# Kernel optimization log

Measured on AMD Instinct MI355X. Metric: run time of the kernel, lower is better.

Reference implementation:

```python
import jax, jax.numpy as jnp
import numpy as np
from jax import lax

B, C, H, W = 32, 256, 56, 56

def _conv(x, w, stride, groups=1, pad='VALID'):
    return lax.conv_general_dilated(x, w, (stride, stride), pad,
                                    feature_group_count=groups,
                                    dimension_numbers=('NCHW', 'OIHW', 'NCHW'))

def _ln(x, g, b, eps=1e-5):
    mu = jnp.mean(x, -1, keepdims=True)
    var = jnp.mean((x - mu) ** 2, -1, keepdims=True)
    return (x - mu) * lax.rsqrt(var + eps) * g + b

def setup_inputs() -> dict:
    key = jax.random.key(0)
    ks = jax.random.split(key, 16)
    s = 0.02
    Ch = C // 2
    d = {}
    d['x'] = jax.random.normal(ks[0], (B, C, H, W), jnp.float32)
    d['Wq'] = jax.random.normal(ks[1], (C, C), jnp.float32) * s;  d['bq'] = jnp.zeros((C,), jnp.float32)
    d['Wk'] = jax.random.normal(ks[2], (C, C), jnp.float32) * s;  d['bk'] = jnp.zeros((C,), jnp.float32)
    d['Wv'] = jax.random.normal(ks[3], (C, C), jnp.float32) * s;  d['bv'] = jnp.zeros((C,), jnp.float32)
    d['sr1_w'] = jax.random.normal(ks[4], (C, C, 8, 8), jnp.float32) * s; d['sr1_b'] = jnp.zeros((C,), jnp.float32)
    d['ln1_g'] = jnp.ones((C,), jnp.float32); d['ln1_b'] = jnp.zeros((C,), jnp.float32)
    d['sr2_w'] = jax.random.normal(ks[5], (C, C, 4, 4), jnp.float32) * s; d['sr2_b'] = jnp.zeros((C,), jnp.float32)
    d['ln2_g'] = jnp.ones((C,), jnp.float32); d['ln2_b'] = jnp.zeros((C,), jnp.float32)
    d['Wkv1'] = jax.random.normal(ks[6], (C, C), jnp.float32) * s; d['bkv1'] = jnp.zeros((C,), jnp.float32)
    d['Wkv2'] = jax.random.normal(ks[7], (C, C), jnp.float32) * s; d['bkv2'] = jnp.zeros((C,), jnp.float32)
    d['lc1_w'] = jax.random.normal(ks[8], (Ch, 1, 3, 3), jnp.float32) * s; d['lc1_b'] = jnp.zeros((Ch,), jnp.float32)
    d['lc2_w'] = jax.random.normal(ks[9], (Ch, 1, 3, 3), jnp.float32) * s; d['lc2_b'] = jnp.zeros((Ch,), jnp.float32)
    d['rp_w'] = jax.random.normal(ks[10], (C, C), jnp.float32) * s;  d['rp_b'] = jnp.zeros((C,), jnp.float32)
    d['rp12_w'] = jax.random.normal(ks[11], (C, C), jnp.float32) * s; d['rp12_b'] = jnp.zeros((C,), jnp.float32)
    d['dw_w'] = jax.random.normal(ks[12], (C, 2), jnp.float32) * 0.5  # Conv3d (2,1,1) depthwise, no bias
    return d

def reference(x, Wq, bq, Wk, bk, Wv, bv, sr1_w, sr1_b, ln1_g, ln1_b,
              sr2_w, sr2_b, ln2_g, ln2_b, Wkv1, bkv1, Wkv2, bkv2,
              lc1_w, lc1_b, lc2_w, lc2_b, rp_w, rp_b, rp12_w, rp12_b, dw_w):
    Bx, Cc, h, w = x.shape
    N = h * w
    Ch = Cc // 2
    xt = x.reshape(Bx, Cc, N).transpose(0, 2, 1)                 # [B,N,C]
    q = jax.nn.softmax(xt @ Wq + bq, axis=-1)                    # softmax over channels
    q1, q2 = q[..., :Ch], q[..., Ch:]

    # spatial-reduction branches (conv -> LN -> GELU)
    x1 = _conv(x, sr1_w, 8) + sr1_b[:, None, None]               # [B,C,7,7]
    x1 = jax.nn.gelu(_ln(x1.reshape(Bx, Cc, -1).transpose(0, 2, 1), ln1_g, ln1_b), approximate=False)
    x2 = _conv(x, sr2_w, 4) + sr2_b[:, None, None]               # [B,C,14,14]
    x2 = jax.nn.gelu(_ln(x2.reshape(Bx, Cc, -1).transpose(0, 2, 1), ln2_g, ln2_b), approximate=False)

    def branch(xr, Wkv, bkv, lc_w, lc_b, qh, hh):
        kv = (xr @ Wkv + bkv).reshape(Bx, -1, 2, Ch)
        k = jax.nn.softmax(kv[:, :, 0], axis=1)                  # softmax over reduced tokens
        v = kv[:, :, 1]
        vsp = v.transpose(0, 2, 1).reshape(Bx, Ch, hh, hh)
        v = v + (_conv(vsp, lc_w, 1, groups=Ch, pad='SAME') + lc_b[:, None, None]).reshape(Bx, Ch, -1).transpose(0, 2, 1)
        ctx = jnp.einsum('bnk,bnv->bkv', k, v)                   # [B,Ch,Ch]
        return jnp.einsum('bnk,bkv->bnv', qh, ctx)               # [B,N,Ch]

    a1 = branch(x1, Wkv1, bkv1, lc1_w, lc1_b, q1, 7)
    a2 = branch(x2, Wkv2, bkv2, lc2_w, lc2_b, q2, 14)
    eff2 = jnp.concatenate([a1, a2], axis=-1)                    # [B,N,C]
    eff2 = jnp.einsum('bni,oi->bon', eff2, rp12_w).reshape(Bx, Cc, h, w) + rp12_b[None, :, None, None]

    # global efficient-attention branch
    keys = jax.nn.softmax(xt @ Wk + bk, axis=1)                  # softmax over tokens
    values = xt @ Wv + bv
    ctx = jnp.einsum('bnk,bnv->bkv', keys, values)               # [B,C,C]
    att = jnp.einsum('bnk,bkv->bnv', q, ctx)                     # [B,N,C]
    eff = jnp.einsum('bni,oi->bon', att, rp_w).reshape(Bx, Cc, h, w) + rp_b[None, :, None, None]

    # Conv3d (2,1,1) depthwise merge over the two branches
    out = eff * dw_w[:, 0][None, :, None, None] + eff2 * dw_w[:, 1][None, :, None, None]
    return out
```

## Files before the change

kernel.cpp:

```cpp
#include <hip/hip_runtime.h>
#include <hip/hip_bf16.h>
#include <math.h>

#define B_ 32
#define H_ 56
#define W_ 56
#define N_ 3136
#define NT_ 100352

typedef short short8 __attribute__((ext_vector_type(8)));
typedef float f32x4 __attribute__((ext_vector_type(4)));

__device__ __forceinline__ unsigned short f2b(float f){
  union { float f; unsigned u; } v; v.f = f;
  return (unsigned short)((v.u + 0x7FFFu + ((v.u>>16)&1u)) >> 16);
}

#define LDSW(row, bo) ((unsigned)((row)*128 + ((bo) ^ (((row)&7)<<4))))

__device__ __forceinline__ short8 ldfrag(const char* base, int row, int kk){
  return *(const short8*)(base + LDSW(row, kk*2));
}
__device__ __forceinline__ f32x4 mfma16(short8 a, short8 b, f32x4 c){
  return __builtin_amdgcn_mfma_f32_16x16x32_bf16(a, b, c, 0, 0, 0);
}

__global__ void prep_kernel(const float* __restrict__ Wq, const float* __restrict__ Wk,
                            const float* __restrict__ Wv, const float* __restrict__ Wkv1,
                            const float* __restrict__ Wkv2, const float* __restrict__ sr1w,
                            const float* __restrict__ sr2w, const float* __restrict__ rpw,
                            const float* __restrict__ rpb, const float* __restrict__ rp12w,
                            const float* __restrict__ rp12b, const float* __restrict__ dww,
                            unsigned short* WqT, unsigned short* WkT, unsigned short* WvT,
                            unsigned short* Wkv1T, unsigned short* Wkv2T,
                            unsigned short* srw1, unsigned short* srw2,
                            unsigned short* Acomb, float* bias_out)
{
  int idx = blockIdx.x*256 + threadIdx.x;
  const int total = 5*65536 + 4194304 + 1048576 + 131072 + 256;
  for (int i = idx; i < total; i += gridDim.x*256) {
    int j = i;
    if (j < 5*65536) {
      int w = j >> 16, e = j & 65535;
      int o = e >> 8, c = e & 255;
      const float* src = (w==0)?Wq:(w==1)?Wk:(w==2)?Wv:(w==3)?Wkv1:Wkv2;
      unsigned short* dst = (w==0)?WqT:(w==1)?WkT:(w==2)?WvT:(w==3)?Wkv1T:Wkv2T;
      dst[o*256+c] = f2b(src[c*256+o]);
      continue;
    }
    j -= 5*65536;
    if (j < 4194304) {
      int o = j >> 14, rem = j & 16383, pos = rem >> 8, c = rem & 255;
      srw1[j] = f2b(sr1w[o*16384 + c*64 + pos]);
      continue;
    }
    j -= 4194304;
    if (j < 1048576) {
      int o = j >> 12, rem = j & 4095, pos = rem >> 8, c = rem & 255;
      srw2[j] = f2b(sr2w[o*4096 + c*16 + pos]);
      continue;
    }
    j -= 1048576;
    if (j < 131072) {
      int o = j >> 9, i2 = j & 511;
      float v = (i2 < 256) ? dww[o*2+0]*rpw[o*256+i2]
                           : dww[o*2+1]*rp12w[o*256+(i2-256)];
      Acomb[o*512+i2] = f2b(v);
      continue;
    }
    j -= 131072;
    bias_out[j] = dww[j*2+0]*rpb[j] + dww[j*2+1]*rp12b[j];
  }
}

__global__ void transpose_kernel(const float* __restrict__ x, unsigned short* __restrict__ xt)
{
  __shared__ float tile[64][65];
  int bn = blockIdx.x; int b = bn / 49; int n0 = (bn - b*49)*64;
  int c0 = blockIdx.y*64;
  int t = threadIdx.x;
  {
    int cl = t >> 2, nq = t & 3;
    const float* src = x + ((size_t)(b*256 + c0 + cl))*N_ + n0 + nq*16;
#pragma unroll
    for (int j = 0; j < 4; j++){
      float4 v = *(const float4*)(src + j*4);
      tile[cl][nq*16 + j*4 + 0] = v.x;
      tile[cl][nq*16 + j*4 + 1] = v.y;
      tile[cl][nq*16 + j*4 + 2] = v.z;
      tile[cl][nq*16 + j*4 + 3] = v.w;
    }
  }
  __syncthreads();
  {
    int nl = t >> 2, cq = t & 3;
    unsigned short pk[16];
#pragma unroll
    for (int j=0;j<16;j++) pk[j] = f2b(tile[cq*16+j][nl]);
    unsigned short* dst = xt + ((size_t)(b*N_ + n0 + nl))*256 + c0 + cq*16;
    *(uint4*)dst = *(uint4*)&pk[0];
    *(uint4*)(dst+8) = *(uint4*)&pk[8];
  }
}

__global__ __launch_bounds__(256,2) void qkv_kernel(
    const unsigned short* __restrict__ xt,
    const unsigned short* __restrict__ WqT, const unsigned short* __restrict__ WkT,
    const unsigned short* __restrict__ WvT,
    const float* __restrict__ bq, const float* __restrict__ bk, const float* __restrict__ bv,
    unsigned short* __restrict__ qbuf, unsigned short* __restrict__ KexpT,
    unsigned short* __restrict__ VT, float* __restrict__ s_k)
{
  __shared__ __align__(16) char smem[32768 + 32768 + 1024];
  char* At = smem;
  char* Bt = smem + 32768;
  float* redbuf = (float*)(smem + 65536);
  const int t = threadIdx.x, wave = t>>6, lane = t&63, l15 = lane&15, l4 = lane>>4;
  const int r0 = blockIdx.x*64;
  const int b = r0 / N_;
  const int nl0 = r0 - b*N_;

#pragma unroll
  for (int c4=0;c4<4;c4++)
#pragma unroll
    for (int j=0;j<2;j++){
      int chunk = j*256 + t; int row = chunk>>3, c8 = chunk&7;
      *(uint4*)(At + c4*8192 + LDSW(row, c8*16)) =
          *(const uint4*)(xt + (size_t)(r0+row)*256 + c4*64 + c8*8);
    }
  __syncthreads();

  for (int mat=0; mat<3; mat++){
    const unsigned short* BT = (mat==0)?WqT:(mat==1)?WkT:WvT;
    const float* bias = (mat==0)?bq:(mat==1)?bk:bv;
    const f32x4 vzero = {0.f,0.f,0.f,0.f};
    f32x4 acc[4][4];
#pragma unroll
    for (int i=0;i<4;i++)
#pragma unroll
      for (int j=0;j<4;j++) acc[i][j] = vzero;

    for (int k0c=0;k0c<4;k0c++){
#pragma unroll
      for (int j=0;j<8;j++){
        int chunk = j*256 + t; int row = chunk>>3, c8 = chunk&7;
        *(uint4*)(Bt + LDSW(row, c8*16)) = *(const uint4*)(BT + (size_t)row*256 + k0c*64 + c8*8);
      }
      __syncthreads();
#pragma unroll
      for (int ks=0;ks<2;ks++){
        short8 af[4], bfr[4];
#pragma unroll
        for (int mi=0;mi<4;mi++) af[mi]  = ldfrag(At + k0c*8192, mi*16 + l15, ks*32 + l4*8);
#pragma unroll
        for (int ni=0;ni<4;ni++) bfr[ni] = ldfrag(Bt, wave*64 + ni*16 + l15, ks*32 + l4*8);
#pragma unroll
        for (int mi=0;mi<4;mi++)
#pragma unroll
          for (int ni=0;ni<4;ni++)
            acc[mi][ni] = mfma16(af[mi], bfr[ni], acc[mi][ni]);
      }
      __syncthreads();
    }

    float bb4[4];
#pragma unroll
    for (int ni=0;ni<4;ni++) bb4[ni] = bias[wave*64 + ni*16 + l15];

    if (mat == 0) {
      float rs[4][4];
#pragma unroll
      for (int mi=0;mi<4;mi++)
#pragma unroll
        for (int r=0;r<4;r++) rs[mi][r] = 0.f;
#pragma unroll
      for (int mi=0;mi<4;mi++)
#pragma unroll
        for (int ni=0;ni<4;ni++)
#pragma unroll
          for (int r=0;r<4;r++){
            float e = expf(acc[mi][ni][r] + bb4[ni]);
            acc[mi][ni][r] = e;
            rs[mi][r] += e;
          }
#pragma unroll
      for (int mi=0;mi<4;mi++)
#pragma unroll
        for (int r=0;r<4;r++){
          float s = rs[mi][r];
          s += __shfl_xor(s, 1); s += __shfl_xor(s, 2);
          s += __shfl_xor(s, 4); s += __shfl_xor(s, 8);
          rs[mi][r] = s;
        }
      if (l15 == 0){
#pragma unroll
        for (int mi=0;mi<4;mi++)
#pragma unroll
          for (int r=0;r<4;r++)
            redbuf[wave*64 + mi*16 + l4*4 + r] = rs[mi][r];
      }
      __syncthreads();
      unsigned short* qb = (unsigned short*)Bt;
#pragma unroll
      for (int mi=0;mi<4;mi++)
#pragma unroll
        for (int r=0;r<4;r++){
          int rr = mi*16 + l4*4 + r;
          float stot = redbuf[rr] + redbuf[64+rr] + redbuf[128+rr] + redbuf[192+rr];
          float inv = 1.0f / stot;
#pragma unroll
          for (int ni=0;ni<4;ni++)
            qb[rr*256 + wave*64 + ni*16 + l15] = f2b(acc[mi][ni][r] * inv);
        }
      __syncthreads();
#pragma unroll
      for (int j=0;j<8;j++){
        int chunk = j*256 + t;
        int row = chunk >> 5, c8 = chunk & 31;
        *(uint4*)(qbuf + (size_t)(r0+row)*256 + c8*8) = *(const uint4*)(qb + row*256 + c8*8);
      }
      __syncthreads();
    } else {
      float cs[4] = {0.f,0.f,0.f,0.f};
#pragma unroll
      for (int mi=0;mi<4;mi++)
#pragma unroll
        for (int ni=0;ni<4;ni++)
#pragma unroll
          for (int r=0;r<4;r++){
            float v = acc[mi][ni][r] + bb4[ni];
            if (mat == 1){ v = expf(v); cs[ni] += v; }
            int row = mi*16 + l4*4 + r;
            int col = wave*64 + ni*16 + l15;
            *(unsigned short*)(Bt + LDSW(col, row*2)) = f2b(v);
          }
      if (mat == 1){
#pragma unroll
        for (int ni=0;ni<4;ni++){
          float s = cs[ni];
          s += __shfl_xor(s, 16);
          s += __shfl_xor(s, 32);
          if (lane < 16) atomicAdd(&s_k[b*256 + wave*64 + ni*16 + lane], s);
        }
      }
      __syncthreads();
      unsigned short* ot = (mat==1) ? KexpT : VT;
#pragma unroll
      for (int j=0;j<8;j++){
        int chunk = j*256 + t;
        int c = chunk >> 3, n8 = chunk & 7;
        *(uint4*)(ot + ((size_t)b*256 + c)*N_ + nl0 + n8*8) = *(const uint4*)(Bt + LDSW(c, n8*16));
      }
      __syncthreads();
    }
  }
}

template<int MODE>
__global__ __launch_bounds__(256,2) void tile128_kernel(
    const unsigned short* __restrict__ Ag, const unsigned short* __restrict__ Bg,
    unsigned short* __restrict__ outg, float* __restrict__ part)
{
  __shared__ __align__(16) char smem[32768];
  char* At = smem; char* Bt = smem + 16384;
  const int b = blockIdx.x;
  const int mt = (MODE==0) ? (blockIdx.y >> 1) : blockIdx.y;
  const int nt = (MODE==0) ? (blockIdx.y & 1)  : blockIdx.z;
  const int it0 = (MODE==0) ? blockIdx.z*7 : 0;
  const int it1 = (MODE==0) ? it0+7 : 8;
  const int t = threadIdx.x;
  const int wave = t>>6, lane = t&63, l15 = lane&15, l4 = lane>>4;
  const int wm = (wave>>1)*64, wn = (wave&1)*64;
  const size_t astr = (MODE==0) ? (size_t)N_ : (size_t)512;
  const unsigned short* A  = (MODE==0) ? (Ag + ((size_t)b*256 + mt*128)*N_) : (Ag + (size_t)mt*128*512);
  const unsigned short* Bv = (MODE==0) ? (Bg + ((size_t)b*256 + nt*128)*N_) : (Bg + ((size_t)b*256 + nt*128)*512);
  const f32x4 vzero = {0.f,0.f,0.f,0.f};
  f32x4 acc[4][4];
#pragma unroll
  for (int i=0;i<4;i++)
#pragma unroll
    for (int j=0;j<4;j++) acc[i][j] = vzero;

  for (int it=it0; it<it1; it++){
    const int k0 = it*64;
#pragma unroll
    for (int j=0;j<4;j++){
      int chunk = j*256 + t; int row = chunk>>3, c8 = chunk&7;
      *(uint4*)(At + LDSW(row, c8*16)) = *(const uint4*)(A + (size_t)row*astr + k0 + c8*8);
    }
#pragma unroll
    for (int j=0;j<4;j++){
      int chunk = j*256 + t; int row = chunk>>3, c8 = chunk&7;
      *(uint4*)(Bt + LDSW(row, c8*16)) = *(const uint4*)(Bv + (size_t)row*astr + k0 + c8*8);
    }
    __syncthreads();
#pragma unroll
    for (int ks=0;ks<2;ks++){
      short8 af[4], bfr[4];
#pragma unroll
      for (int mi=0;mi<4;mi++) af[mi]  = ldfrag(At, wm + mi*16 + l15, ks*32 + l4*8);
#pragma unroll
      for (int ni=0;ni<4;ni++) bfr[ni] = ldfrag(Bt, wn + ni*16 + l15, ks*32 + l4*8);
#pragma unroll
      for (int mi=0;mi<4;mi++)
#pragma unroll
        for (int ni=0;ni<4;ni++)
          acc[mi][ni] = mfma16(af[mi], bfr[ni], acc[mi][ni]);
    }
    __syncthreads();
  }
  if (MODE==0){
    const int sk = blockIdx.z;
#pragma unroll
    for (int mi=0;mi<4;mi++)
#pragma unroll
      for (int r=0;r<4;r++){
        int kg = mt*128 + wm + mi*16 + l4*4 + r;
        size_t basep = (((size_t)sk*B_ + b)*256 + kg)*256 + nt*128 + wn;
#pragma unroll
        for (int ni=0;ni<4;ni++)
          part[basep + ni*16 + l15] = acc[mi][ni][r];
      }
  } else {
#pragma unroll
    for (int mi=0;mi<4;mi++)
#pragma unroll
      for (int r=0;r<4;r++){
        int og = mt*128 + wm + mi*16 + l4*4 + r;
#pragma unroll
        for (int ni=0;ni<4;ni++)
          outg[(size_t)b*65536 + (size_t)og*256 + nt*128 + wn + ni*16 + l15] = f2b(acc[mi][ni][r]);
      }
  }
}

__global__ __launch_bounds__(256) void ctxred_kernel(
    const float* __restrict__ part, const float* __restrict__ s_k,
    unsigned short* __restrict__ ctxcomb)
{
  int e = (blockIdx.x*256 + threadIdx.x)*4;
  int b = e >> 16; int rem = e & 65535; int kg = rem >> 8; int col = rem & 255;
  float4 s = {0.f,0.f,0.f,0.f};
#pragma unroll
  for (int sk=0; sk<7; sk++){
    float4 p = *(const float4*)(part + ((((size_t)sk*B_ + b)*256 + kg)<<8) + col);
    s.x += p.x; s.y += p.y; s.z += p.z; s.w += p.w;
  }
  float inv = 1.0f / s_k[b*256 + kg];
  unsigned short pk[4] = {f2b(s.x*inv), f2b(s.y*inv), f2b(s.z*inv), f2b(s.w*inv)};
  *(uint2*)(ctxcomb + ((size_t)b*256 + kg)*512 + col) = *(uint2*)&pk[0];
}

template<int S, int OW, int KW, int NSK, int MPB, int KTOT>
__device__ __forceinline__ void srconv_body(
    const unsigned short* __restrict__ xt, const unsigned short* __restrict__ wbf,
    float* __restrict__ part, int bid, char* At, char* Bt)
{
  const int KCH = KTOT / NSK;
  const int Mtot = B_*MPB;
  const int sk = bid % NSK, tile = bid / NSK;
  const int t = threadIdx.x, wave = t>>6, lane = t&63, l15 = lane&15, l4 = lane>>4;
  const f32x4 vzero = {0.f,0.f,0.f,0.f};
  f32x4 acc[4][4];
#pragma unroll
  for (int i=0;i<4;i++)
#pragma unroll
    for (int j=0;j<4;j++) acc[i][j] = vzero;

  size_t abase[2];
#pragma unroll
  for (int j=0;j<2;j++){
    int chunk = j*256 + t;
    int row = chunk >> 3, c8 = chunk & 7;
    int rowc = tile*64 + row; if (rowc > Mtot-1) rowc = Mtot-1;
    int b = rowc / MPB; int m = rowc - b*MPB;
    int p = m / OW; int q = m - p*OW;
    abase[j] = ((size_t)b*N_ + (size_t)(S*p)*W_ + S*q)*256 + c8*8;
  }

  for (int kt = 0; kt < KCH; kt += 64){
    const int k0 = sk*KCH + kt;
    const int pos = k0 >> 8, cc = k0 & 255;
    const int dy = pos / KW, dx = pos - dy*KW;
    const size_t off = (size_t)(dy*W_ + dx)*256 + cc;
#pragma unroll
    for (int j=0;j<2;j++){
      int chunk = j*256 + t; int row = chunk>>3, c8 = chunk&7;
      *(uint4*)(At + LDSW(row, c8*16)) = *(const uint4*)(xt + abase[j] + off);
    }
#pragma unroll
    for (int j=0;j<8;j++){
      int chunk = j*256 + t; int row = chunk>>3, c8 = chunk&7;
      *(uint4*)(Bt + LDSW(row, c8*16)) = *(const uint4*)(wbf + (size_t)row*KTOT + k0 + c8*8);
    }
    __syncthreads();
#pragma unroll
    for (int ks=0;ks<2;ks++){
      short8 af[4], bfr[4];
#pragma unroll
      for (int mi=0;mi<4;mi++) af[mi]  = ldfrag(At, mi*16 + l15, ks*32 + l4*8);
#pragma unroll
      for (int ni=0;ni<4;ni++) bfr[ni] = ldfrag(Bt, wave*64 + ni*16 + l15, ks*32 + l4*8);
#pragma unroll
      for (int mi=0;mi<4;mi++)
#pragma unroll
        for (int ni=0;ni<4;ni++)
          acc[mi][ni] = mfma16(af[mi], bfr[ni], acc[mi][ni]);
    }
    __syncthreads();
  }
#pragma unroll
  for (int mi=0;mi<4;mi++)
#pragma unroll
    for (int r=0;r<4;r++){
      int row = tile*64 + mi*16 + l4*4 + r;
      if (row < Mtot){
        size_t basep = ((size_t)sk*Mtot + row)*256;
#pragma unroll
        for (int ni=0;ni<4;ni++)
          part[basep + wave*64 + ni*16 + l15] = acc[mi][ni][r];
      }
    }
}

__global__ __launch_bounds__(256,4) void srconv_both_kernel(
    const unsigned short* __restrict__ xt, const unsigned short* __restrict__ srw1,
    const unsigned short* __restrict__ srw2, float* __restrict__ x1part,
    float* __restrict__ x2part)
{
  __shared__ __align__(16) char smem[8192 + 32768];
  if (blockIdx.x < 400)
    srconv_body<8,7,8,16,49,16384>(xt, srw1, x1part, blockIdx.x, smem, smem+8192);
  else
    srconv_body<4,14,4,4,196,4096>(xt, srw2, x2part, blockIdx.x-400, smem, smem+8192);
}

__device__ __forceinline__ void lngelu_body(
    const float* __restrict__ part, const float* __restrict__ srb,
    const float* __restrict__ g, const float* __restrict__ bb,
    unsigned short* __restrict__ out, int M, int nsk, int Mtot, int bid,
    float* red)
{
  int b = bid / M, m = bid - b*M;
  int c = threadIdx.x;
  float v = srb[c];
  for (int s=0;s<nsk;s++) v += part[((size_t)s*Mtot + b*M + m)*256 + c];
  int wave = c>>6, lane = c&63;
  float s1 = v;
  s1 += __shfl_xor(s1,1); s1 += __shfl_xor(s1,2); s1 += __shfl_xor(s1,4);
  s1 += __shfl_xor(s1,8); s1 += __shfl_xor(s1,16); s1 += __shfl_xor(s1,32);
  if (lane==0) red[wave] = s1;
  __syncthreads();
  float mu = (red[0]+red[1]+red[2]+red[3]) * (1.0f/256.0f);
  float d = v - mu;
  float s2 = d*d;
  s2 += __shfl_xor(s2,1); s2 += __shfl_xor(s2,2); s2 += __shfl_xor(s2,4);
  s2 += __shfl_xor(s2,8); s2 += __shfl_xor(s2,16); s2 += __shfl_xor(s2,32);
  if (lane==0) red[4+wave] = s2;
  __syncthreads();
  float var = (red[4]+red[5]+red[6]+red[7]) * (1.0f/256.0f);
  float y = d * rsqrtf(var + 1e-5f) * g[c] + bb[c];
  float ge = 0.5f * y * (1.0f + erff(y * 0.70710678118654752f));
  out[((size_t)b*M + m)*256 + c] = f2b(ge);
}

__global__ __launch_bounds__(256) void lngelu_both_kernel(
    const float* __restrict__ x1part, const float* __restrict__ x2part,
    const float* __restrict__ sr1b, const float* __restrict__ sr2b,
    const float* __restrict__ ln1g, const float* __restrict__ ln1b,
    const float* __restrict__ ln2g, const float* __restrict__ ln2b,
    unsigned short* __restrict__ x1g, unsigned short* __restrict__ x2g)
{
  __shared__ float red[8];
  if (blockIdx.x < 1568)
    lngelu_body(x1part, sr1b, ln1g, ln1b, x1g, 49, 16, 1568, blockIdx.x, red);
  else
    lngelu_body(x2part, sr2b, ln2g, ln2b, x2g, 196, 4, 6272, blockIdx.x-1568, red);
}

__global__ __launch_bounds__(256,2) void kv_both_kernel(
    const unsigned short* __restrict__ x1g, const unsigned short* __restrict__ Wkv1T,
    const float* __restrict__ bkv1, float* __restrict__ kexp1, float* __restrict__ vraw1,
    const unsigned short* __restrict__ x2g, const unsigned short* __restrict__ Wkv2T,
    const float* __restrict__ bkv2, float* __restrict__ kexp2, float* __restrict__ vraw2)
{
  __shared__ __align__(16) char smem[8192 + 32768];
  char* At = smem; char* Bt = smem + 8192;
  const unsigned short* A; const unsigned short* BT; const float* bias;
  float* kexp; float* vraw; int r0; int R;
  if (blockIdx.x < 25){ A=x1g; BT=Wkv1T; bias=bkv1; kexp=kexp1; vraw=vraw1; r0=blockIdx.x*64; R=1568; }
  else { A=x2g; BT=Wkv2T; bias=bkv2; kexp=kexp2; vraw=vraw2; r0=(blockIdx.x-25)*64; R=6272; }
  const int t = threadIdx.x, wave = t>>6, lane = t&63, l15 = lane&15, l4 = lane>>4;
  const f32x4 vzero = {0.f,0.f,0.f,0.f};
  f32x4 acc[4][4];
#pragma unroll
  for (int i=0;i<4;i++)
#pragma unroll
    for (int j=0;j<4;j++) acc[i][j] = vzero;

  for (int k0 = 0; k0 < 256; k0 += 64) {
#pragma unroll
    for (int j = 0; j < 2; j++){
      int chunk = j*256 + t;
      int row = chunk >> 3, c8 = chunk & 7;
      int rg = r0 + row; if (rg > R-1) rg = R-1;
      *(uint4*)(At + LDSW(row, c8*16)) = *(const uint4*)(A + (size_t)rg*256 + k0 + c8*8);
    }
#pragma unroll
    for (int j = 0; j < 8; j++){
      int chunk = j*256 + t;
      int row = chunk >> 3, c8 = chunk & 7;
      *(uint4*)(Bt + LDSW(row, c8*16)) = *(const uint4*)(BT + (size_t)row*256 + k0 + c8*8);
    }
    __syncthreads();
#pragma unroll
    for (int ks = 0; ks < 2; ks++){
      short8 af[4], bfr[4];
#pragma unroll
      for (int mi=0;mi<4;mi++) af[mi]  = ldfrag(At, mi*16 + l15, ks*32 + l4*8);
#pragma unroll
      for (int ni=0;ni<4;ni++) bfr[ni] = ldfrag(Bt, wave*64 + ni*16 + l15, ks*32 + l4*8);
#pragma unroll
      for (int mi=0;mi<4;mi++)
#pragma unroll
        for (int ni=0;ni<4;ni++)
          acc[mi][ni] = mfma16(af[mi], bfr[ni], acc[mi][ni]);
    }
    __syncthreads();
  }
  float bb4[4];
#pragma unroll
  for (int ni=0;ni<4;ni++) bb4[ni] = bias[wave*64 + ni*16 + l15];
#pragma unroll
  for (int mi=0;mi<4;mi++)
#pragma unroll
    for (int ni=0;ni<4;ni++)
#pragma unroll
      for (int r=0;r<4;r++){
        int rg = r0 + mi*16 + l4*4 + r;
        if (rg < R){
          int col = wave*64 + ni*16 + l15;
          float v = acc[mi][ni][r] + bb4[ni];
          if (col < 128) kexp[(size_t)rg*128 + col] = expf(v);
          else           vraw[(size_t)rg*128 + (col-128)] = v;
        }
      }
}

__device__ __forceinline__ void dwconv_body(
    const float* __restrict__ vraw, const float* __restrict__ lcw,
    const float* __restrict__ lcb, float* __restrict__ vmod, int M, int OW, int idx)
{
  int ch = idx & 127; int rest = idx >> 7; int m = rest % M; int b = rest / M;
  if (b >= B_) return;
  int py = m / OW, px = m - py*OW;
  float acc = vraw[((size_t)b*M + m)*128 + ch] + lcb[ch];
#pragma unroll
  for (int dy=0;dy<3;dy++)
#pragma unroll
    for (int dx=0;dx<3;dx++){
      int yy = py+dy-1, xx = px+dx-1;
      if (yy>=0 && yy<OW && xx>=0 && xx<OW)
        acc += vraw[((size_t)b*M + yy*OW+xx)*128 + ch] * lcw[ch*9 + dy*3 + dx];
    }
  vmod[((size_t)b*M + m)*128 + ch] = acc;
}

__global__ __launch_bounds__(256) void dwconv_both_kernel(
    const float* __restrict__ vraw1, const float* __restrict__ lc1w,
    const float* __restrict__ lc1b, float* __restrict__ vmod1,
    const float* __restrict__ vraw2, const float* __restrict__ lc2w,
    const float* __restrict__ lc2b, float* __restrict__ vmod2)
{
  int gid = blockIdx.x*256 + threadIdx.x;
  if (blockIdx.x < 784) dwconv_body(vraw1, lc1w, lc1b, vmod1, 49, 7, gid);
  else dwconv_body(vraw2, lc2w, lc2b, vmod2, 196, 14, gid - 784*256);
}

__global__ __launch_bounds__(512) void ctxbr_both_kernel(
    const float* __restrict__ kexp1, const float* __restrict__ vmod1,
    const float* __restrict__ kexp2, const float* __restrict__ vmod2,
    unsigned short* __restrict__ ctxcomb)
{
  const int b = blockIdx.x;
  int kc = blockIdx.y;
  const float* kexp; const float* vmod; int M, BR;
  if (kc < 32){ kexp = kexp1; vmod = vmod1; M = 49; BR = 0; }
  else { kexp = kexp2; vmod = vmod2; M = 196; BR = 1; kc -= 32; }
  const int t = threadIdx.x;
  const int kl = t >> 7, j = t & 127;
  const int kk = kc*4 + kl;
  const float* kp = kexp + (size_t)b*M*128 + kk;
  const float* vp = vmod + (size_t)b*M*128 + j;
  float acc = 0.f, s = 0.f;
  for (int m = 0; m < M; m++){
    float kv = kp[(size_t)m*128];
    s += kv;
    acc += kv * vp[(size_t)m*128];
  }
  const int krow = BR ? (128+kk) : kk;
  unsigned short* dst = ctxcomb + ((size_t)b*256 + krow)*512;
  const int wbase = BR ? 384 : 256;
  const int zbase = BR ? 256 : 384;
  dst[wbase + j] = f2b(acc / s);
  dst[zbase + j] = 0;
}

__global__ __launch_bounds__(256,2) void final_kernel(
    const unsigned short* __restrict__ Gmat, const unsigned short* __restrict__ qbuf,
    const float* __restrict__ bias_out, float* __restrict__ out)
{
  __shared__ __align__(16) char smem[16384 + 8192];
  char* At = smem; char* Bt = smem + 16384;
  const int b = blockIdx.x, ot = blockIdx.y, nt = blockIdx.z;
  const int t = threadIdx.x, wave = t>>6, lane = t&63, l15 = lane&15, l4 = lane>>4;
  const int wm = (wave>>1)*64, wn = (wave&1)*32;
  const unsigned short* A  = Gmat + ((size_t)b*256 + ot*128)*256;
  const unsigned short* Bq = qbuf + ((size_t)b*N_ + nt*64)*256;
  const f32x4 vzero = {0.f,0.f,0.f,0.f};
  f32x4 acc[4][2];
#pragma unroll
  for (int i=0;i<4;i++){ acc[i][0] = vzero; acc[i][1] = vzero; }

  for (int k0=0;k0<256;k0+=64){
#pragma unroll
    for (int j=0;j<4;j++){
      int chunk = j*256 + t; int row = chunk>>3, c8 = chunk&7;
      *(uint4*)(At + LDSW(row, c8*16)) = *(const uint4*)(A + (size_t)row*256 + k0 + c8*8);
    }
#pragma unroll
    for (int j=0;j<2;j++){
      int chunk = j*256 + t; int row = chunk>>3, c8 = chunk&7;
      *(uint4*)(Bt + LDSW(row, c8*16)) = *(const uint4*)(Bq + (size_t)row*256 + k0 + c8*8);
    }
    __syncthreads();
#pragma unroll
    for (int ks=0;ks<2;ks++){
      short8 af[4], bfr[2];
#pragma unroll
      for (int mi=0;mi<4;mi++) af[mi]  = ldfrag(At, wm + mi*16 + l15, ks*32 + l4*8);
#pragma unroll
      for (int ni=0;ni<2;ni++) bfr[ni] = ldfrag(Bt, wn + ni*16 + l15, ks*32 + l4*8);
#pragma unroll
      for (int mi=0;mi<4;mi++)
#pragma unroll
        for (int ni=0;ni<2;ni++)
          acc[mi][ni] = mfma16(af[mi], bfr[ni], acc[mi][ni]);
    }
    __syncthreads();
  }
#pragma unroll
  for (int mi=0;mi<4;mi++)
#pragma unroll
    for (int r=0;r<4;r++){
      int o = ot*128 + wm + mi*16 + l4*4 + r;
      float bo = bias_out[o];
#pragma unroll
      for (int ni=0;ni<2;ni++){
        int n = nt*64 + wn + ni*16 + l15;
        out[((size_t)b*256 + o)*N_ + n] = acc[mi][ni][r] + bo;
      }
    }
}

extern "C" void kernel_launch(void* const* d_in, const int* in_sizes, int n_in,
                              void* d_out, int out_size, void* d_ws, size_t ws_size,
                              hipStream_t stream)
{
  const float* x     = (const float*)d_in[0];
  const float* Wq    = (const float*)d_in[1];
  const float* bq    = (const float*)d_in[2];
  const float* Wk    = (const float*)d_in[3];
  const float* bk    = (const float*)d_in[4];
  const float* Wv    = (const float*)d_in[5];
  const float* bv    = (const float*)d_in[6];
  const float* sr1w  = (const float*)d_in[7];
  const float* sr1b  = (const float*)d_in[8];
  const float* ln1g  = (const float*)d_in[9];
  const float* ln1b  = (const float*)d_in[10];
  const float* sr2w  = (const float*)d_in[11];
  const float* sr2b  = (const float*)d_in[12];
  const float* ln2g  = (const float*)d_in[13];
  const float* ln2b  = (const float*)d_in[14];
  const float* Wkv1  = (const float*)d_in[15];
  const float* bkv1  = (const float*)d_in[16];
  const float* Wkv2  = (const float*)d_in[17];
  const float* bkv2  = (const float*)d_in[18];
  const float* lc1w  = (const float*)d_in[19];
  const float* lc1b  = (const float*)d_in[20];
  const float* lc2w  = (const float*)d_in[21];
  const float* lc2b  = (const float*)d_in[22];
  const float* rpw   = (const float*)d_in[23];
  const float* rpb   = (const float*)d_in[24];
  const float* rp12w = (const float*)d_in[25];
  const float* rp12b = (const float*)d_in[26];
  const float* dww   = (const float*)d_in[27];

  char* ws = (char*)d_ws;
  size_t off = 0;
  auto take = [&](size_t n)->char*{ char* p = ws + off; off += (n + 255) & ~(size_t)255; return p; };

  unsigned short* WqT   = (unsigned short*)take(131072);
  unsigned short* WkT   = (unsigned short*)take(131072);
  unsigned short* WvT   = (unsigned short*)take(131072);
  unsigned short* Wkv1T = (unsigned short*)take(131072);
  unsigned short* Wkv2T = (unsigned short*)take(131072);
  unsigned short* srw1  = (unsigned short*)take(8388608);
  unsigned short* srw2  = (unsigned short*)take(2097152);
  unsigned short* Acomb = (unsigned short*)take(262144);
  float* bias_out = (float*)take(1024);
  float* s_k      = (float*)take(32768);
  char* regionA = take(51380224);
  unsigned short* qbuf = (unsigned short*)take(51380224);
  char* regionK = take(51380224);
  char* regionV = take(51380224);
  if (off > ws_size) return;

  unsigned short* xt    = (unsigned short*)regionA;
  unsigned short* KexpT = (unsigned short*)regionK;
  float* x1part = (float*)regionK;
  float* x2part = (float*)(regionK + 25690112);
  unsigned short* VT = (unsigned short*)regionV;
  unsigned short* Gmat = (unsigned short*)regionV;
  unsigned short* x1g  = (unsigned short*)(regionV + 4194304);
  unsigned short* x2g  = (unsigned short*)(regionV + 4997120);
  float* kexp1 = (float*)(regionV + 8208384);
  float* vraw1 = (float*)(regionV + 9011200);
  float* vmod1 = (float*)(regionV + 9814016);
  float* kexp2 = (float*)(regionV + 10616832);
  float* vraw2 = (float*)(regionV + 13828096);
  float* vmod2 = (float*)(regionV + 17039360);
  unsigned short* ctxcomb = (unsigned short*)d_out;
  float* ctxpart = (float*)((char*)d_out + 8388608);

  hipMemsetAsync(s_k, 0, 32768, stream);
  prep_kernel<<<8192, 256, 0, stream>>>(Wq, Wk, Wv, Wkv1, Wkv2, sr1w, sr2w,
                                        rpw, rpb, rp12w, rp12b, dww,
                                        WqT, WkT, WvT, Wkv1T, Wkv2T, srw1, srw2,
                                        Acomb, bias_out);
  transpose_kernel<<<dim3(1568,4), 256, 0, stream>>>(x, xt);
  qkv_kernel<<<1568, 256, 0, stream>>>(xt, WqT, WkT, WvT, bq, bk, bv,
                                       qbuf, KexpT, VT, s_k);
  tile128_kernel<0><<<dim3(32,4,7), 256, 0, stream>>>(KexpT, VT, nullptr, ctxpart);
  ctxred_kernel<<<2048, 256, 0, stream>>>(ctxpart, s_k, ctxcomb);
  srconv_both_kernel<<<792, 256, 0, stream>>>(xt, srw1, srw2, x1part, x2part);
  lngelu_both_kernel<<<7840, 256, 0, stream>>>(x1part, x2part, sr1b, sr2b,
                                               ln1g, ln1b, ln2g, ln2b, x1g, x2g);
  kv_both_kernel<<<123, 256, 0, stream>>>(x1g, Wkv1T, bkv1, kexp1, vraw1,
                                          x2g, Wkv2T, bkv2, kexp2, vraw2);
  dwconv_both_kernel<<<3920, 256, 0, stream>>>(vraw1, lc1w, lc1b, vmod1,
                                               vraw2, lc2w, lc2b, vmod2);
  ctxbr_both_kernel<<<dim3(32,64), 512, 0, stream>>>(kexp1, vmod1, kexp2, vmod2, ctxcomb);
  tile128_kernel<1><<<dim3(32,2,2), 256, 0, stream>>>(Acomb, ctxcomb, Gmat, nullptr);
  final_kernel<<<dim3(32,2,49), 256, 0, stream>>>(Gmat, qbuf, bias_out, (float*)d_out);
}
```

Before: 468.3 us.

## Retile QKV projection to 128x128 blocks and defer q-softmax normalization to final kernel

The QKV projection kernel changes from 64-row tiles covering all 256 output columns to 128x128 tiles in a 2D grid, with A and B streamed per k-chunk and less shared memory so three blocks can fit per CU. Because a block no longer sees a full q row, the softmax row sums go to a global s_q buffer through atomics, and the division is folded into the final output kernel's epilogue. expf is replaced by __expf. The aim is more reuse per MFMA tile and higher occupancy, at the cost of extra atomics, the s_q memset, unnormalized bf16 q storage, and slightly lower exp precision.

```diff
diff --git a/kernel.cpp b/kernel.cpp
--- a/kernel.cpp
+++ b/kernel.cpp
@@ -17,6 +17,7 @@
 }
 
 #define LDSW(row, bo) ((unsigned)((row)*128 + ((bo) ^ (((row)&7)<<4))))
+#define TSW(row, bo) ((unsigned)((row)*256 + ((bo) ^ (((row)&15)<<4))))
 
 __device__ __forceinline__ short8 ldfrag(const char* base, int row, int kk){
   return *(const short8*)(base + LDSW(row, kk*2));
@@ -103,32 +104,22 @@
   }
 }
 
-__global__ __launch_bounds__(256,2) void qkv_kernel(
+__global__ __launch_bounds__(256,3) void qkv2_kernel(
     const unsigned short* __restrict__ xt,
     const unsigned short* __restrict__ WqT, const unsigned short* __restrict__ WkT,
     const unsigned short* __restrict__ WvT,
     const float* __restrict__ bq, const float* __restrict__ bk, const float* __restrict__ bv,
     unsigned short* __restrict__ qbuf, unsigned short* __restrict__ KexpT,
-    unsigned short* __restrict__ VT, float* __restrict__ s_k)
-{
-  __shared__ __align__(16) char smem[32768 + 32768 + 1024];
-  char* At = smem;
-  char* Bt = smem + 32768;
-  float* redbuf = (float*)(smem + 65536);
+    unsigned short* __restrict__ VT, float* __restrict__ s_q, float* __restrict__ s_k)
+{
+  __shared__ __align__(16) char smem[32768];
+  char* At = smem; char* Bt = smem + 16384;
+  const int nt = blockIdx.x, tile = blockIdx.y;
   const int t = threadIdx.x, wave = t>>6, lane = t&63, l15 = lane&15, l4 = lane>>4;
-  const int r0 = blockIdx.x*64;
-  const int b = r0 / N_;
-  const int nl0 = r0 - b*N_;
-
-#pragma unroll
-  for (int c4=0;c4<4;c4++)
-#pragma unroll
-    for (int j=0;j<2;j++){
-      int chunk = j*256 + t; int row = chunk>>3, c8 = chunk&7;
-      *(uint4*)(At + c4*8192 + LDSW(row, c8*16)) =
-          *(const uint4*)(xt + (size_t)(r0+row)*256 + c4*64 + c8*8);
-    }
-  __syncthreads();
+  const int wm = (wave>>1)*64, wn = (wave&1)*64;
+  const int r0 = tile*128;
+  const int b0 = r0 / N_;
+  const int nl0 = r0 - b0*N_;
 
   for (int mat=0; mat<3; mat++){
     const unsigned short* BT = (mat==0)?WqT:(mat==1)?WkT:WvT;
@@ -140,20 +131,27 @@
 #pragma unroll
       for (int j=0;j<4;j++) acc[i][j] = vzero;
 
+#pragma unroll
     for (int k0c=0;k0c<4;k0c++){
-#pragma unroll
-      for (int j=0;j<8;j++){
+      const int k0 = k0c*64;
+#pragma unroll
+      for (int j=0;j<4;j++){
         int chunk = j*256 + t; int row = chunk>>3, c8 = chunk&7;
-        *(uint4*)(Bt + LDSW(row, c8*16)) = *(const uint4*)(BT + (size_t)row*256 + k0c*64 + c8*8);
+        *(uint4*)(At + LDSW(row, c8*16)) = *(const uint4*)(xt + (size_t)(r0+row)*256 + k0 + c8*8);
+      }
+#pragma unroll
+      for (int j=0;j<4;j++){
+        int chunk = j*256 + t; int row = chunk>>3, c8 = chunk&7;
+        *(uint4*)(Bt + LDSW(row, c8*16)) = *(const uint4*)(BT + (size_t)(nt*128+row)*256 + k0 + c8*8);
       }
       __syncthreads();
 #pragma unroll
       for (int ks=0;ks<2;ks++){
         short8 af[4], bfr[4];
 #pragma unroll
-        for (int mi=0;mi<4;mi++) af[mi]  = ldfrag(At + k0c*8192, mi*16 + l15, ks*32 + l4*8);
-#pragma unroll
-        for (int ni=0;ni<4;ni++) bfr[ni] = ldfrag(Bt, wave*64 + ni*16 + l15, ks*32 + l4*8);
+        for (int mi=0;mi<4;mi++) af[mi]  = ldfrag(At, wm + mi*16 + l15, ks*32 + l4*8);
+#pragma unroll
+        for (int ni=0;ni<4;ni++) bfr[ni] = ldfrag(Bt, wn + ni*16 + l15, ks*32 + l4*8);
 #pragma unroll
         for (int mi=0;mi<4;mi++)
 #pragma unroll
@@ -165,7 +163,7 @@
 
     float bb4[4];
 #pragma unroll
-    for (int ni=0;ni<4;ni++) bb4[ni] = bias[wave*64 + ni*16 + l15];
+    for (int ni=0;ni<4;ni++) bb4[ni] = bias[nt*128 + wn + ni*16 + l15];
 
     if (mat == 0) {
       float rs[4][4];
@@ -179,7 +177,7 @@
         for (int ni=0;ni<4;ni++)
 #pragma unroll
           for (int r=0;r<4;r++){
-            float e = expf(acc[mi][ni][r] + bb4[ni]);
+            float e = __expf(acc[mi][ni][r] + bb4[ni]);
             acc[mi][ni][r] = e;
             rs[mi][r] += e;
           }
@@ -197,27 +195,24 @@
         for (int mi=0;mi<4;mi++)
 #pragma unroll
           for (int r=0;r<4;r++)
-            redbuf[wave*64 + mi*16 + l4*4 + r] = rs[mi][r];
-      }
+            atomicAdd(&s_q[r0 + wm + mi*16 + l4*4 + r], rs[mi][r]);
+      }
+#pragma unroll
+      for (int mi=0;mi<4;mi++)
+#pragma unroll
+        for (int ni=0;ni<4;ni++)
+#pragma unroll
+          for (int r=0;r<4;r++){
+            int row = wm + mi*16 + l4*4 + r;
+            int colb = (wn + ni*16 + l15)*2;
+            *(unsigned short*)(smem + TSW(row, colb)) = f2b(acc[mi][ni][r]);
+          }
       __syncthreads();
-      unsigned short* qb = (unsigned short*)Bt;
-#pragma unroll
-      for (int mi=0;mi<4;mi++)
-#pragma unroll
-        for (int r=0;r<4;r++){
-          int rr = mi*16 + l4*4 + r;
-          float stot = redbuf[rr] + redbuf[64+rr] + redbuf[128+rr] + redbuf[192+rr];
-          float inv = 1.0f / stot;
-#pragma unroll
-          for (int ni=0;ni<4;ni++)
-            qb[rr*256 + wave*64 + ni*16 + l15] = f2b(acc[mi][ni][r] * inv);
-        }
-      __syncthreads();
 #pragma unroll
       for (int j=0;j<8;j++){
-        int chunk = j*256 + t;
-        int row = chunk >> 5, c8 = chunk & 31;
-        *(uint4*)(qbuf + (size_t)(r0+row)*256 + c8*8) = *(const uint4*)(qb + row*256 + c8*8);
+        int chunk = j*256 + t; int row = chunk>>4, c16 = chunk&15;
+        uint4 v = *(const uint4*)(smem + TSW(row, c16*16));
+        *(uint4*)(qbuf + (size_t)(r0+row)*256 + nt*128 + c16*8) = v;
       }
       __syncthreads();
     } else {
@@ -229,27 +224,30 @@
 #pragma unroll
           for (int r=0;r<4;r++){
             float v = acc[mi][ni][r] + bb4[ni];
-            if (mat == 1){ v = expf(v); cs[ni] += v; }
-            int row = mi*16 + l4*4 + r;
-            int col = wave*64 + ni*16 + l15;
-            *(unsigned short*)(Bt + LDSW(col, row*2)) = f2b(v);
+            if (mat == 1){ v = __expf(v); cs[ni] += v; }
+            int c = wn + ni*16 + l15;
+            int row = wm + mi*16 + l4*4 + r;
+            *(unsigned short*)(smem + TSW(c, row*2)) = f2b(v);
           }
       if (mat == 1){
+        int bbw = (r0 + wm) / N_;
 #pragma unroll
         for (int ni=0;ni<4;ni++){
           float s = cs[ni];
           s += __shfl_xor(s, 16);
           s += __shfl_xor(s, 32);
-          if (lane < 16) atomicAdd(&s_k[b*256 + wave*64 + ni*16 + lane], s);
+          if (lane < 16) atomicAdd(&s_k[bbw*256 + nt*128 + wn + ni*16 + lane], s);
         }
       }
       __syncthreads();
       unsigned short* ot = (mat==1) ? KexpT : VT;
 #pragma unroll
       for (int j=0;j<8;j++){
-        int chunk = j*256 + t;
-        int c = chunk >> 3, n8 = chunk & 7;
-        *(uint4*)(ot + ((size_t)b*256 + c)*N_ + nl0 + n8*8) = *(const uint4*)(Bt + LDSW(c, n8*16));
+        int chunk = j*256 + t; int c = chunk>>4, n16 = chunk&15;
+        uint4 v = *(const uint4*)(smem + TSW(c, n16*16));
+        int nl = nl0 + n16*8; int bb = b0;
+        if (nl >= N_){ bb++; nl -= N_; }
+        *(uint4*)(ot + ((size_t)bb*256 + nt*128 + c)*N_ + nl) = v;
       }
       __syncthreads();
     }
@@ -541,7 +539,7 @@
         if (rg < R){
           int col = wave*64 + ni*16 + l15;
           float v = acc[mi][ni][r] + bb4[ni];
-          if (col < 128) kexp[(size_t)rg*128 + col] = expf(v);
+          if (col < 128) kexp[(size_t)rg*128 + col] = __expf(v);
           else           vraw[(size_t)rg*128 + (col-128)] = v;
         }
       }
@@ -608,7 +606,8 @@
 
 __global__ __launch_bounds__(256,2) void final_kernel(
     const unsigned short* __restrict__ Gmat, const unsigned short* __restrict__ qbuf,
-    const float* __restrict__ bias_out, float* __restrict__ out)
+    const float* __restrict__ bias_out, const float* __restrict__ s_q,
+    float* __restrict__ out)
 {
   __shared__ __align__(16) char smem[16384 + 8192];
   char* At = smem; char* Bt = smem + 16384;
@@ -649,6 +648,10 @@
     }
     __syncthreads();
   }
+  float iq[2];
+#pragma unroll
+  for (int ni=0;ni<2;ni++)
+    iq[ni] = 1.0f / s_q[(size_t)b*N_ + nt*64 + wn + ni*16 + l15];
 #pragma unroll
   for (int mi=0;mi<4;mi++)
 #pragma unroll
@@ -658,7 +661,7 @@
 #pragma unroll
       for (int ni=0;ni<2;ni++){
         int n = nt*64 + wn + ni*16 + l15;
-        out[((size_t)b*256 + o)*N_ + n] = acc[mi][ni][r] + bo;
+        out[((size_t)b*256 + o)*N_ + n] = acc[mi][ni][r]*iq[ni] + bo;
       }
     }
 }
@@ -710,6 +713,7 @@
   unsigned short* Acomb = (unsigned short*)take(262144);
   float* bias_out = (float*)take(1024);
   float* s_k      = (float*)take(32768);
+  float* s_q      = (float*)take(401408);
   char* regionA = take(51380224);
   unsigned short* qbuf = (unsigned short*)take(51380224);
   char* regionK = take(51380224);
@@ -733,14 +737,14 @@
   unsigned short* ctxcomb = (unsigned short*)d_out;
   float* ctxpart = (float*)((char*)d_out + 8388608);
 
-  hipMemsetAsync(s_k, 0, 32768, stream);
+  hipMemsetAsync(s_k, 0, 32768 + 401408, stream);
   prep_kernel<<<8192, 256, 0, stream>>>(Wq, Wk, Wv, Wkv1, Wkv2, sr1w, sr2w,
                                         rpw, rpb, rp12w, rp12b, dww,
                                         WqT, WkT, WvT, Wkv1T, Wkv2T, srw1, srw2,
                                         Acomb, bias_out);
   transpose_kernel<<<dim3(1568,4), 256, 0, stream>>>(x, xt);
-  qkv_kernel<<<1568, 256, 0, stream>>>(xt, WqT, WkT, WvT, bq, bk, bv,
-                                       qbuf, KexpT, VT, s_k);
+  qkv2_kernel<<<dim3(2,784), 256, 0, stream>>>(xt, WqT, WkT, WvT, bq, bk, bv,
+                                               qbuf, KexpT, VT, s_q, s_k);
   tile128_kernel<0><<<dim3(32,4,7), 256, 0, stream>>>(KexpT, VT, nullptr, ctxpart);
   ctxred_kernel<<<2048, 256, 0, stream>>>(ctxpart, s_k, ctxcomb);
   srconv_both_kernel<<<792, 256, 0, stream>>>(xt, srw1, srw2, x1part, x2part);
@@ -752,5 +756,5 @@
                                                vraw2, lc2w, lc2b, vmod2);
   ctxbr_both_kernel<<<dim3(32,64), 512, 0, stream>>>(kexp1, vmod1, kexp2, vmod2, ctxcomb);
   tile128_kernel<1><<<dim3(32,2,2), 256, 0, stream>>>(Acomb, ctxcomb, Gmat, nullptr);
-  final_kernel<<<dim3(32,2,49), 256, 0, stream>>>(Gmat, qbuf, bias_out, (float*)d_out);
-}
+  final_kernel<<<dim3(32,2,49), 256, 0, stream>>>(Gmat, qbuf, bias_out, s_q, (float*)d_out);
+}
```

After: 598.8 us. 27.9% more time.
